# Performance work log

Hardware: AMD Instinct MI355X
Metric: run time of the kernel (lower is better)

Reference implementation:

```python
import jax, jax.numpy as jnp
import numpy as np
from jax import lax

H_IMG = 128; W_IMG = 128; C_IN = 200; NCLS = 16
N0 = H_IMG * W_IMG; N1 = 4096; N2 = 1024
K = 16  # neighbors(15) + 1 self loop, as in __init__
EPS = 1e-5
SLOPE = 0.01  # LeakyReLU default


def _leaky(x):
    return jnp.where(x >= 0, x, SLOPE * x)


def _bn1d(H, g, b):
    # BatchNorm1d in training mode: batch stats over node dim
    mu = H.mean(0)
    var = H.var(0)
    return (H - mu) * lax.rsqrt(var + EPS) * g + b


def _bn2d(x, g, b):
    mu = x.mean((0, 2, 3), keepdims=True)
    var = x.var((0, 2, 3), keepdims=True)
    return (x - mu) * lax.rsqrt(var + EPS) * g[None, :, None, None] + b[None, :, None, None]


def _ssconv(x, g, b, pw, pb, dw, db):
    # BN -> 1x1 pointwise conv -> LeakyReLU -> depthwise 5x5 conv -> LeakyReLU
    y = _bn2d(x, g, b)
    y = lax.conv_general_dilated(y, pw, (1, 1), 'SAME', dimension_numbers=('NCHW', 'OIHW', 'NCHW')) + pb[None, :, None, None]
    y = _leaky(y)
    c = dw.shape[0]
    y = lax.conv_general_dilated(y, dw, (1, 1), 'SAME', feature_group_count=c, dimension_numbers=('NCHW', 'OIHW', 'NCHW')) + db[None, :, None, None]
    return _leaky(y)


def _gcn(H, g, b, wt, bt, wo, bo, nbr):
    # GCNLayer_PyG, neighbors>0 branch. nbr: [N, K] neighbor indices (col), center broadcast (row)
    Hn = _bn1d(H, g, b)
    th = Hn @ wt + bt            # [N, 128]
    out = Hn @ wo + bo           # [N, F]
    A = jax.nn.sigmoid(jnp.einsum('nkd,nd->nk', th[nbr], th))  # sigmoid(<theta[col], theta[row]>)
    A = jax.nn.softmax(A, axis=1)                              # softmax over K neighbors
    agg = jnp.einsum('nk,nkf->nf', A, out[nbr])                # weighted neighbor aggregate
    return _leaky(agg), A


def _forward(x, hg, hb, hpw, hpb, hdw, hdb,
             e0_g, e0_b, e0_wt, e0_bt, e0_wo, e0_bo,
             e1_g, e1_b, e1_wt, e1_bt, e1_wo, e1_bo,
             d0_g, d0_b, d0_wt, d0_bt, d0_wo, d0_bo,
             tg, tb, tpw, tpb, tdw, tdb, ws, wb,
             S0, S1, Shat0, Shat1, nbr_a, nbr_b):
    x4 = x.transpose(2, 0, 1)[None]                 # [1, C, H, W]
    h0 = _ssconv(x4, hg, hb, hpw, hpb, hdw, hdb)    # [1, 128, H, W]
    H = h0[0].transpose(1, 2, 0).reshape(N0, -1)    # [N0, 128]
    enc0 = H
    H = Shat0 @ H                                   # pool to [N1, 128]
    H, A0 = _gcn(H, e0_g, e0_b, e0_wt, e0_bt, e0_wo, e0_bo, nbr_a)  # [N1, 64]
    enc1 = H
    H = Shat1 @ H                                   # pool to [N2, 64]
    H, A1 = _gcn(H, e1_g, e1_b, e1_wt, e1_bt, e1_wo, e1_bo, nbr_b)  # [N2, 32]
    # decoder
    H = S1 @ H                                      # unpool [N1, 32]
    H = jnp.concatenate([H, enc1], axis=-1)         # [N1, 96]
    H, Ad = _gcn(H, d0_g, d0_b, d0_wt, d0_bt, d0_wo, d0_bo, nbr_a)  # [N1, 64]
    H = S0 @ H                                      # unpool [N0, 64]
    H = jnp.concatenate([H, enc0], axis=-1)         # [N0, 192]
    t = H.reshape(1, H_IMG, W_IMG, -1).transpose(0, 3, 1, 2)
    f = _ssconv(t, tg, tb, tpw, tpb, tdw, tdb)      # [1, 128, H, W]
    f = f[0].transpose(1, 2, 0).reshape(N0, -1)
    Y = jax.nn.softmax(f @ ws + wb, axis=-1)        # [N0, NCLS]
    return Y


def setup_inputs() -> dict:
    key = jax.random.key(0)
    cnt = [0]
    def rn(shape, s=0.05):
        cnt[0] += 1
        return jax.random.normal(jax.random.fold_in(key, cnt[0]), shape, jnp.float32) * s
    x = rn((H_IMG, W_IMG, C_IN), 1.0)
    # balanced hierarchical assignment matrices (one-hot rows)
    S0 = jnp.zeros((N0, N1), jnp.float32).at[jnp.arange(N0), jnp.arange(N0) // (N0 // N1)].set(1.0)
    S1 = jnp.zeros((N1, N2), jnp.float32).at[jnp.arange(N1), jnp.arange(N1) // (N1 // N2)].set(1.0)
    Shat0 = (S0 / S0.sum(0, keepdims=True)).T
    Shat1 = (S1 / S1.sum(0, keepdims=True)).T
    # positions: pixel grid pooled through Shat (as in HiGCN.__init__)
    gx, gy = jnp.meshgrid(jnp.arange(H_IMG), jnp.arange(W_IMG), indexing='ij')
    pos = jnp.stack([gx, gy], -1).reshape(N0, 2).astype(jnp.float32)
    posA = Shat0 @ pos
    posB = Shat1 @ posA
    def knn(p):
        d = ((p[:, None, :] - p[None, :, :]) ** 2).sum(-1)
        return jnp.argsort(d, axis=1)[:, :K].astype(jnp.int32)  # self included (loop=True)
    nbr_a = knn(posA)  # [N1, K], used by enc0 and dec0
    nbr_b = knn(posB)  # [N2, K], used by enc1
    inp = dict(x=x, S0=S0, S1=S1, Shat0=Shat0, Shat1=Shat1, nbr_a=nbr_a, nbr_b=nbr_b)
    inp.update(hg=jnp.ones(C_IN), hb=jnp.zeros(C_IN), hpw=rn((128, C_IN, 1, 1)),
               hpb=jnp.zeros(128), hdw=rn((128, 1, 5, 5)), hdb=jnp.zeros(128))
    for tag, ci, co in (('e0', 128, 64), ('e1', 64, 32), ('d0', 96, 64)):
        inp[tag + '_g'] = jnp.ones(ci); inp[tag + '_b'] = jnp.zeros(ci)
        inp[tag + '_wt'] = rn((ci, 128)); inp[tag + '_bt'] = jnp.zeros(128)
        inp[tag + '_wo'] = rn((ci, co)); inp[tag + '_bo'] = jnp.zeros(co)
    inp.update(tg=jnp.ones(192), tb=jnp.zeros(192), tpw=rn((128, 192, 1, 1)),
               tpb=jnp.zeros(128), tdw=rn((128, 1, 5, 5)), tdb=jnp.zeros(128))
    inp.update(ws=rn((128, NCLS)), wb=jnp.zeros(NCLS))
    return inp


def reference(x, hg, hb, hpw, hpb, hdw, hdb,
              e0_g, e0_b, e0_wt, e0_bt, e0_wo, e0_bo,
              e1_g, e1_b, e1_wt, e1_bt, e1_wo, e1_bo,
              d0_g, d0_b, d0_wt, d0_bt, d0_wo, d0_bo,
              tg, tb, tpw, tpb, tdw, tdb, ws, wb,
              S0, S1, Shat0, Shat1, nbr_a, nbr_b):
    return _forward(x, hg, hb, hpw, hpb, hdw, hdb,
                    e0_g, e0_b, e0_wt, e0_bt, e0_wo, e0_bo,
                    e1_g, e1_b, e1_wt, e1_bt, e1_wo, e1_bo,
                    d0_g, d0_b, d0_wt, d0_bt, d0_wo, d0_bo,
                    tg, tb, tpw, tpb, tdw, tdb, ws, wb,
                    S0, S1, Shat0, Shat1, nbr_a, nbr_b)
```

## Files before the change

### kernel.cpp

```cpp
#include <hip/hip_runtime.h>
#include <hip/hip_bf16.h>
#include <math.h>

using bf16 = __hip_bfloat16;

#define H_IMG 128
#define W_IMG 128
#define C_IN  200
#define NCLS  16
#define N0    16384
#define N1    4096
#define N2    1024
#define KNB   16
#define EPS   1e-5f
#define SLOPE 0.01f

__device__ __forceinline__ float ldf(const float* p, long i) { return p[i]; }
__device__ __forceinline__ float ldf(const bf16* p, long i) { return __bfloat162float(p[i]); }
__device__ __forceinline__ float leaky(float v) { return v >= 0.f ? v : SLOPE * v; }

__device__ __forceinline__ float4 ld4(const float* p, long i) {
    return *reinterpret_cast<const float4*>(p + i);
}
__device__ __forceinline__ float4 ld4(const bf16* p, long i) {
    const ushort4 u = *reinterpret_cast<const ushort4*>(reinterpret_cast<const unsigned short*>(p) + i);
    float4 r;
    r.x = __uint_as_float((unsigned)u.x << 16);
    r.y = __uint_as_float((unsigned)u.y << 16);
    r.z = __uint_as_float((unsigned)u.z << 16);
    r.w = __uint_as_float((unsigned)u.w << 16);
    return r;
}

__device__ __forceinline__ int block_detect(const unsigned short* __restrict__ x) {
    __shared__ int cnt_s;
    if (threadIdx.x == 0) cnt_s = 0;
    __syncthreads();
    int cnt = 0;
    for (int i = threadIdx.x; i < 4096; i += blockDim.x) {
        unsigned short e = (unsigned short)((x[i] >> 7) & 0xFF);
        if (e >= 0xC0) cnt++;
    }
#pragma unroll
    for (int off = 32; off > 0; off >>= 1) cnt += __shfl_xor(cnt, off, 64);
    if ((threadIdx.x & 63) == 0) atomicAdd(&cnt_s, cnt);
    __syncthreads();
    return cnt_s > 32 ? 1 : 0;
}

__global__ __launch_bounds__(256) void bnx_kernel(const void* __restrict__ X, float2* __restrict__ part,
                                                  int* __restrict__ dflag) {
    int fl = block_detect((const unsigned short*)X);
    if (blockIdx.x == 0 && threadIdx.x == 0) *dflag = fl;
    int b = blockIdx.x, t = threadIdx.x;
    if (t >= C_IN) return;
    float s = 0.f, s2 = 0.f;
    if (fl) {
        const float* p = (const float*)X + (long)b * 64 * C_IN + t;
        for (int r = 0; r < 64; r++) { float v = p[(long)r * C_IN]; s += v; s2 += v * v; }
    } else {
        const bf16* p = (const bf16*)X + (long)b * 64 * C_IN + t;
        for (int r = 0; r < 64; r++) { float v = __bfloat162float(p[(long)r * C_IN]); s += v; s2 += v * v; }
    }
    part[(long)t * 256 + b] = make_float2(s, s2);
}

__device__ __forceinline__ void alphabeta_ld(const float2* __restrict__ partA, int npA, int splitC,
                                             const float2* __restrict__ partB, int npB,
                                             int Ci, float Pinv, const void* g, const void* b_,
                                             int flag, float* al, float* be) {
    int t = threadIdx.x;
    if (t < Ci) {
        const float2* src = (t < splitC) ? partA + (long)t * npA : partB + (long)(t - splitC) * npB;
        int np = (t < splitC) ? npA : npB;
        float s = 0.f, s2 = 0.f;
        const float4* p4 = (const float4*)src;
        for (int i = 0; i < (np >> 1); i++) { float4 v = p4[i]; s += v.x + v.z; s2 += v.y + v.w; }
        float mu = s * Pinv;
        float var = s2 * Pinv - mu * mu;
        float gv = flag ? ((const float*)g)[t] : __bfloat162float(((const bf16*)g)[t]);
        float bv = flag ? ((const float*)b_)[t] : __bfloat162float(((const bf16*)b_)[t]);
        float a = rsqrtf(var + EPS) * gv;
        al[t] = a;
        be[t] = bv - mu * a;
    }
    __syncthreads();
}

template <typename TW>
__device__ __forceinline__ void foldL_body(const TW* __restrict__ W, const TW* __restrict__ bias,
                                           const float* __restrict__ al, const float* __restrict__ be,
                                           float* __restrict__ Wf, float* __restrict__ Bf,
                                           int Ci, int Co, int omajor, int j) {
    int t = threadIdx.x;
    float acc = 0.f;
    for (int c = t; c < Ci; c += 256) {
        float w = omajor ? ldf(W, (long)j * Ci + c) : ldf(W, (long)c * Co + j);
        Wf[(long)c * Co + j] = w * al[c];
        acc += w * be[c];
    }
    __shared__ float red[256];
    red[t] = acc; __syncthreads();
    for (int k = 128; k > 0; k >>= 1) { if (t < k) red[t] += red[t + k]; __syncthreads(); }
    if (t == 0) Bf[j] = ldf(bias, (long)j) + red[0];
}

__global__ __launch_bounds__(256) void bnfold_kernel(const float2* partA, int npA, int splitC,
                                                     const float2* partB, int npB, int P,
                                                     const void* g, const void* b_,
                                                     const void* Wt, const void* bias,
                                                     float* Wf, float* Bf, int Ci, int Co, int omajor,
                                                     const int* dflag) {
    __shared__ float al[256], be[256];
    int flag = *dflag;
    alphabeta_ld(partA, npA, splitC, partB, npB, Ci, 1.f / (float)P, g, b_, flag, al, be);
    if (flag) foldL_body<float>((const float*)Wt, (const float*)bias, al, be, Wf, Bf, Ci, Co, omajor, blockIdx.x);
    else foldL_body<bf16>((const bf16*)Wt, (const bf16*)bias, al, be, Wf, Bf, Ci, Co, omajor, blockIdx.x);
}

__global__ __launch_bounds__(256) void bnfold2_kernel(const float2* partA, int npA, int splitC,
                                                      const float2* partB, int npB, int P,
                                                      const void* g, const void* b_,
                                                      const void* W1, const void* b1,
                                                      const void* W2, const void* b2,
                                                      float* Wf1, float* Bf1, float* Wf2, float* Bf2,
                                                      int Ci, int Co1, int Co2, const int* dflag) {
    __shared__ float al[256], be[256];
    int flag = *dflag;
    alphabeta_ld(partA, npA, splitC, partB, npB, Ci, 1.f / (float)P, g, b_, flag, al, be);
    int j = blockIdx.x;
    if (flag) {
        if (j < Co1) foldL_body<float>((const float*)W1, (const float*)b1, al, be, Wf1, Bf1, Ci, Co1, 0, j);
        else foldL_body<float>((const float*)W2, (const float*)b2, al, be, Wf2, Bf2, Ci, Co2, 0, j - Co1);
    } else {
        if (j < Co1) foldL_body<bf16>((const bf16*)W1, (const bf16*)b1, al, be, Wf1, Bf1, Ci, Co1, 0, j);
        else foldL_body<bf16>((const bf16*)W2, (const bf16*)b2, al, be, Wf2, Bf2, Ci, Co2, 0, j - Co1);
    }
}

template <typename T, int ACT>
__device__ __forceinline__ void gemm4_body(const T* __restrict__ In, const float* __restrict__ Wf,
                                           const float* __restrict__ Bf, float* __restrict__ Out,
                                           int Ci, int Co, int blk) {
    int tid = blk * 256 + threadIdx.x;
    int Coq = Co >> 2;
    int n = tid / Coq;
    int j4 = (tid - n * Coq) << 2;
    const T* in = In + (long)n * Ci;
    const float* wp = Wf + j4;
    float4 acc = *reinterpret_cast<const float4*>(Bf + j4);
    for (int c = 0; c < Ci; c += 4) {
        float4 xv = ld4(in, c);
        float4 w0 = *reinterpret_cast<const float4*>(wp + (long)c * Co);
        float4 w1 = *reinterpret_cast<const float4*>(wp + (long)(c + 1) * Co);
        float4 w2 = *reinterpret_cast<const float4*>(wp + (long)(c + 2) * Co);
        float4 w3 = *reinterpret_cast<const float4*>(wp + (long)(c + 3) * Co);
        acc.x += xv.x * w0.x; acc.y += xv.x * w0.y; acc.z += xv.x * w0.z; acc.w += xv.x * w0.w;
        acc.x += xv.y * w1.x; acc.y += xv.y * w1.y; acc.z += xv.y * w1.z; acc.w += xv.y * w1.w;
        acc.x += xv.z * w2.x; acc.y += xv.z * w2.y; acc.z += xv.z * w2.z; acc.w += xv.z * w2.w;
        acc.x += xv.w * w3.x; acc.y += xv.w * w3.y; acc.z += xv.w * w3.z; acc.w += xv.w * w3.w;
    }
// ... 10 lines not shown
    int Coq = Co >> 2;
    int n = tid / Coq;
    int j4 = (tid - n * Coq) << 2;
    const float* ia = InA + (long)(n >> 2) * sA;
    const float* ib = InB + (long)n * sB;
    const float* wp = Wf + j4;
    float4 acc = *reinterpret_cast<const float4*>(Bf + j4);
    for (int c = 0; c < Ci; c += 4) {
        float4 xv = (c < SPLIT) ? *reinterpret_cast<const float4*>(ia + c)
                                : *reinterpret_cast<const float4*>(ib + (c - SPLIT));
        float4 w0 = *reinterpret_cast<const float4*>(wp + (long)c * Co);
        float4 w1 = *reinterpret_cast<const float4*>(wp + (long)(c + 1) * Co);
        float4 w2 = *reinterpret_cast<const float4*>(wp + (long)(c + 2) * Co);
        float4 w3 = *reinterpret_cast<const float4*>(wp + (long)(c + 3) * Co);
        acc.x += xv.x * w0.x; acc.y += xv.x * w0.y; acc.z += xv.x * w0.z; acc.w += xv.x * w0.w;
        acc.x += xv.y * w1.x; acc.y += xv.y * w1.y; acc.z += xv.y * w1.z; acc.w += xv.y * w1.w;
        acc.x += xv.z * w2.x; acc.y += xv.z * w2.y; acc.z += xv.z * w2.z; acc.w += xv.z * w2.w;
        acc.x += xv.w * w3.x; acc.y += xv.w * w3.y; acc.z += xv.w * w3.z; acc.w += xv.w * w3.w;
    }
    if (ACT) { acc.x = leaky(acc.x); acc.y = leaky(acc.y); acc.z = leaky(acc.z); acc.w = leaky(acc.w); }
    *reinterpret_cast<float4*>(Out + (long)n * Co + j4) = acc;
}

__global__ __launch_bounds__(256) void gemm4_dyn_kernel(const void* In, const float* Wf, const float* Bf,
                                                        float* Out, int Ci, int Co, const int* flag) {
    if (*flag) gemm4_body<float, 1>((const float*)In, Wf, Bf, Out, Ci, Co, blockIdx.x);
    else gemm4_body<bf16, 1>((const bf16*)In, Wf, Bf, Out, Ci, Co, blockIdx.x);
}

__global__ __launch_bounds__(256) void gemm2_f32_kernel(const float* In,
                                                        const float* W1, const float* B1, float* O1, int Co1,
                                                        const float* W2, const float* B2, float* O2, int Co2,
                                                        int Ci, int nb1) {
    int b = blockIdx.x;
    if (b < nb1) gemm4_body<float, 0>(In, W1, B1, O1, Ci, Co1, b);
    else gemm4_body<float, 0>(In, W2, B2, O2, Ci, Co2, b - nb1);
}

template <int SPLIT>
__global__ __launch_bounds__(256) void gemm2cat_kernel(const float* InA, int sA, const float* InB, int sB,
                                                       const float* W1, const float* B1, float* O1, int Co1,
                                                       const float* W2, const float* B2, float* O2, int Co2,
                                                       int Ci, int nb1) {
    int b = blockIdx.x;
    if (b < nb1) gemm4cat_body<0, SPLIT>(InA, sA, InB, sB, W1, B1, O1, Ci, Co1, b);
    else gemm4cat_body<0, SPLIT>(InA, sA, InB, sB, W2, B2, O2, Ci, Co2, b - nb1);
}

template <int SPLIT>
__global__ __launch_bounds__(256) void gemmcat_act_kernel(const float* InA, int sA, const float* InB, int sB,
                                                          const float* Wf, const float* Bf, float* Out,
                                                          int Ci, int Co) {
    gemm4cat_body<1, SPLIT>(InA, sA, InB, sB, Wf, Bf, Out, Ci, Co, blockIdx.x);
}

template <typename TW>
__device__ __forceinline__ void dw4_body(const float* __restrict__ In, const TW* __restrict__ dwp,
                                         const TW* __restrict__ dbp, float* __restrict__ Out) {
    __shared__ float wl[25][128];
    __shared__ float bl[128];
    int t = threadIdx.x;
    for (int e = t; e < 25 * 128; e += 256) {
        int o = e / 25, i = e - o * 25;
        wl[i][o] = ldf(dwp, e);
    }
    if (t < 128) bl[t] = ldf(dbp, (long)t);
    __syncthreads();

    int tid = blockIdx.x * 256 + t;
    int o0 = (tid & 31) << 2;
    int p = tid >> 5;
    int h = p >> 7, w = p & 127;
    float4 acc = *reinterpret_cast<const float4*>(&bl[o0]);
#pragma unroll
    for (int dh = -2; dh <= 2; dh++) {
        int hh = h + dh;
        if ((unsigned)hh >= (unsigned)H_IMG) continue;
#pragma unroll
        for (int dv = -2; dv <= 2; dv++) {
            int ww = w + dv;
            if ((unsigned)ww >= (unsigned)W_IMG) continue;
            float4 iv = *reinterpret_cast<const float4*>(&In[(long)(((hh << 7) + ww) << 7) + o0]);
            float4 wv = *reinterpret_cast<const float4*>(&wl[(dh + 2) * 5 + (dv + 2)][o0]);
            acc.x += iv.x * wv.x; acc.y += iv.y * wv.y; acc.z += iv.z * wv.z; acc.w += iv.w * wv.w;
        }
    }
    acc.x = leaky(acc.x); acc.y = leaky(acc.y); acc.z = leaky(acc.z); acc.w = leaky(acc.w);
    *reinterpret_cast<float4*>(&Out[(long)p * 128 + o0]) = acc;
}

__global__ __launch_bounds__(256) void dw4_kernel(const float* In, const void* dwp, const void* dbp,
                                                  float* Out, const int* flag) {
    if (*flag) dw4_body<float>(In, (const float*)dwp, (const float*)dbp, Out);
    else dw4_body<bf16>(In, (const bf16*)dwp, (const bf16*)dbp, Out);
}

__global__ __launch_bounds__(128) void bnpool_kernel(const float* __restrict__ R1f, float* __restrict__ H1b,
                                                     float2* __restrict__ partE0, float2* __restrict__ partTb) {
    int b = blockIdx.x, t = threadIdx.x;
    float s = 0.f, s2 = 0.f;
    float rs = 0.f, rs2 = 0.f;
    const float* base = R1f + (long)b * 64 * 128 + t;
    for (int r = 0; r < 16; r++) {
        const float* rp = base + (long)r * 512;
        float v0 = rp[0], v1 = rp[128], v2 = rp[256], v3 = rp[384];
        float h = 0.25f * (v0 + v1 + v2 + v3);
        H1b[(long)(b * 16 + r) * 128 + t] = h;
        s += h; s2 += h * h;
        rs += v0 + v1 + v2 + v3;
        rs2 += v0 * v0 + v1 * v1 + v2 * v2 + v3 * v3;
    }
    partE0[(long)t * 256 + b] = make_float2(s, s2);
    partTb[(long)t * 256 + b] = make_float2(rs, rs2);
}

template <int MODE>
__global__ __launch_bounds__(256) void attn_fused_kernel(const float* __restrict__ th, const float* __restrict__ outm,
                                                         const int* __restrict__ nbr, float* __restrict__ dst, int co,
                                                         float* __restrict__ H2b,
                                                         float2* __restrict__ partP, float2* __restrict__ partS,
                                                         int snp) {
    int wid = threadIdx.x >> 6, l = threadIdx.x & 63;
    int n = blockIdx.x * 4 + wid;
    float r0 = th[(long)n * 128 + l];
    float r1 = th[(long)n * 128 + 64 + l];
    int mk[KNB];
    float av[KNB];
#pragma unroll
    for (int k = 0; k < KNB; k++) {
        int m = nbr[n * KNB + k];
        mk[k] = m;
        float v = r0 * th[(long)m * 128 + l] + r1 * th[(long)m * 128 + 64 + l];
#pragma unroll
        for (int off = 32; off > 0; off >>= 1) v += __shfl_xor(v, off, 64);
        av[k] = 1.f / (1.f + expf(-v));
    }
    float amax = av[0];
#pragma unroll
    for (int k = 1; k < KNB; k++) amax = fmaxf(amax, av[k]);
    float den = 0.f;
#pragma unroll
    for (int k = 0; k < KNB; k++) { av[k] = expf(av[k] - amax); den += av[k]; }
    float rden = 1.f / den;
    float val = 0.f;
    if (l < co) {
        float acc = 0.f;
#pragma unroll
        for (int k = 0; k < KNB; k++) acc += av[k] * outm[(long)mk[k] * co + l];
        val = leaky(acc * rden);
        dst[(long)n * co + l] = val;
    }
    __shared__ float sm[4][64];
    sm[wid][l] = (l < co) ? val : 0.f;
    __syncthreads();
    if (wid == 0 && l < co) {
        float a = sm[0][l], b = sm[1][l], c = sm[2][l], d = sm[3][l];
        float su = a + b + c + d;
        float sq = a * a + b * b + c * c + d * d;
        if (MODE == 0) {
            float h = 0.25f * su;
            H2b[(long)blockIdx.x * 64 + l] = h;
            partP[(long)l * snp + blockIdx.x] = make_float2(h, h * h);
            partS[(long)l * snp + blockIdx.x] = make_float2(su, sq);
        } else {
            partS[(long)l * snp + blockIdx.x] = make_float2(4.f * su, 4.f * sq);
        }
    }
}

template <typename TW>
__device__ __forceinline__ void cls_body(const float* __restrict__ F, const TW* __restrict__ wsw,
                                         const TW* __restrict__ wb, TW* __restrict__ out) {
    __shared__ float wl[128 * 16];
    int t = threadIdx.x;
    for (int e = t; e < 2048; e += 256) wl[e] = ldf(wsw, (long)e);
    __syncthreads();
    int tid = blockIdx.x * 256 + t;
    int p = tid >> 4;
    int j = tid & 15;
    float acc = ldf(wb, (long)j);
    const float* fp = F + (long)p * 128;
#pragma unroll 8
    for (int c = 0; c < 128; c += 4) {
        float4 fv = *reinterpret_cast<const float4*>(fp + c);
        acc += fv.x * wl[c * 16 + j] + fv.y * wl[(c + 1) * 16 + j]
             + fv.z * wl[(c + 2) * 16 + j] + fv.w * wl[(c + 3) * 16 + j];
    }
    float m = acc;
#pragma unroll
    for (int s = 8; s > 0; s >>= 1) m = fmaxf(m, __shfl_xor(m, s, 16));
    float e = expf(acc - m);
    float d = e;
#pragma unroll
    for (int s = 8; s > 0; s >>= 1) d += __shfl_xor(d, s, 16);
    float r = e / d;
    if constexpr (sizeof(TW) == 2) out[tid] = __float2bfloat16(r);
    else out[tid] = r;
}

__global__ __launch_bounds__(256) void cls_kernel(const float* F, const void* wsw, const void* wb,
                                                  void* out, const int* flag) {
    if (*flag) cls_body<float>(F, (const float*)wsw, (const float*)wb, (float*)out);
    else cls_body<bf16>(F, (const bf16*)wsw, (const bf16*)wb, (bf16*)out);
}

extern "C" void kernel_launch(void* const* d_in, const int* in_sizes, int n_in,
                              void* d_out, int out_size, void* d_ws, size_t ws_size,
                              hipStream_t stream) {
    bool dict = (in_sizes[1] > 1000000);
    int I_x, I_nbr_a, I_nbr_b, I_hg, I_ws, I_e0, I_e1, I_d0, I_tg;
    if (dict) {
        I_x = 0; I_nbr_a = 5; I_nbr_b = 6; I_hg = 7; I_e0 = 13; I_e1 = 19; I_d0 = 25; I_tg = 31; I_ws = 37;
    } else {
        I_x = 0; I_hg = 1; I_e0 = 7; I_e1 = 13; I_d0 = 19; I_tg = 25; I_ws = 31; I_nbr_a = 37; I_nbr_b = 38;
    }
    const void* x    = d_in[I_x];
    const int* nbr_a = (const int*)d_in[I_nbr_a];
    const int* nbr_b = (const int*)d_in[I_nbr_b];
    const void* hg   = d_in[I_hg + 0];
    const void* hb   = d_in[I_hg + 1];
    const void* hpw  = d_in[I_hg + 2];
    const void* hpb  = d_in[I_hg + 3];
    const void* hdw  = d_in[I_hg + 4];
    const void* hdb  = d_in[I_hg + 5];
    const void* e0_g = d_in[I_e0 + 0];
    const void* e0_b = d_in[I_e0 + 1];
    const void* e0_wt= d_in[I_e0 + 2];
    const void* e0_bt= d_in[I_e0 + 3];
    const void* e0_wo= d_in[I_e0 + 4];
    const void* e0_bo= d_in[I_e0 + 5];
    const void* e1_g = d_in[I_e1 + 0];
    const void* e1_b = d_in[I_e1 + 1];
    const void* e1_wt= d_in[I_e1 + 2];
    const void* e1_bt= d_in[I_e1 + 3];
    const void* e1_wo= d_in[I_e1 + 4];
    const void* e1_bo= d_in[I_e1 + 5];
    const void* d0_g = d_in[I_d0 + 0];
    const void* d0_b = d_in[I_d0 + 1];
    const void* d0_wt= d_in[I_d0 + 2];
    const void* d0_bt= d_in[I_d0 + 3];
    const void* d0_wo= d_in[I_d0 + 4];
    const void* d0_bo= d_in[I_d0 + 5];
    const void* tg   = d_in[I_tg + 0];
    const void* tb   = d_in[I_tg + 1];
    const void* tpw  = d_in[I_tg + 2];
    const void* tpb  = d_in[I_tg + 3];
    const void* tdw  = d_in[I_tg + 4];
    const void* tdb  = d_in[I_tg + 5];
    const void* wsw  = d_in[I_ws + 0];
    const void* wb   = d_in[I_ws + 1];

    float* W = (float*)d_ws;
    float*  WF1    = W + 0;
    float*  BF1    = W + 25600;
    float*  WF2    = W + 25728;
    float*  BF2    = W + 33920;
    int*    dflag  = (int*)(W + 33984);
    float2* P_HEAD = (float2*)(W + 34048);
    float2* P_E0   = (float2*)(W + 136448);
    float2* P_E1   = (float2*)(W + 201984);
    float2* P_D0a  = (float2*)(W + 333056);
    float2* P_D0b  = (float2*)(W + 349440);
    float2* P_Ta   = (float2*)(W + 480512);
    float2* P_Tb   = (float2*)(W + 611584);
    float*  R0     = W + 677120;
    float*  R1     = R0 + (long)N0 * 128;
    float*  T1     = R1 + (long)N0 * 128;
    float*  H1b    = T1 + (long)N0 * 128;
    float*  THb    = H1b + (long)N1 * 128;
    float*  OUTb   = THb + (long)N1 * 128;
    float*  ENC1   = OUTb + (long)N1 * 64;
    float*  H2b    = ENC1 + (long)N1 * 64;
    float*  HDb    = H2b + (long)N2 * 64;
    float*  HDEC   = HDb + (long)N2 * 32;

    bnx_kernel<<<256, 256, 0, stream>>>(x, P_HEAD, dflag);
    bnfold_kernel<<<128, 256, 0, stream>>>(P_HEAD, 256, C_IN, P_HEAD, 256, N0,
                                           hg, hb, hpw, hpb, WF1, BF1, C_IN, 128, 1, dflag);
    gemm4_dyn_kernel<<<2048, 256, 0, stream>>>(x, WF1, BF1, R0, C_IN, 128, dflag);
    dw4_kernel<<<2048, 256, 0, stream>>>(R0, hdw, hdb, R1, dflag);
    bnpool_kernel<<<256, 128, 0, stream>>>(R1, H1b, P_E0, P_Tb);
    bnfold2_kernel<<<192, 256, 0, stream>>>(P_E0, 256, 128, P_E0, 256, N1, e0_g, e0_b,
                                            e0_wt, e0_bt, e0_wo, e0_bo,
                                            WF1, BF1, WF2, BF2, 128, 128, 64, dflag);
    gemm2_f32_kernel<<<768, 256, 0, stream>>>(H1b, WF1, BF1, THb, 128, WF2, BF2, OUTb, 64, 128, 512);
    attn_fused_kernel<0><<<1024, 256, 0, stream>>>(THb, OUTb, nbr_a, ENC1, 64, H2b, P_E1, P_D0b, 1024);
    bnfold2_kernel<<<160, 256, 0, stream>>>(P_E1, 1024, 64, P_E1, 1024, N2, e1_g, e1_b,
                                            e1_wt, e1_bt, e1_wo, e1_bo,
                                            WF1, BF1, WF2, BF2, 64, 128, 32, dflag);
    gemm2_f32_kernel<<<160, 256, 0, stream>>>(H2b, WF1, BF1, THb, 128, WF2, BF2, OUTb, 32, 64, 128);
    attn_fused_kernel<1><<<256, 256, 0, stream>>>(THb, OUTb, nbr_b, HDb, 32, nullptr, nullptr, P_D0a, 256);
    bnfold2_kernel<<<192, 256, 0, stream>>>(P_D0a, 256, 32, P_D0b, 1024, N1, d0_g, d0_b,
                                            d0_wt, d0_bt, d0_wo, d0_bo,
                                            WF1, BF1, WF2, BF2, 96, 128, 64, dflag);
    gemm2cat_kernel<32><<<768, 256, 0, stream>>>(HDb, 32, ENC1, 64,
                                                 WF1, BF1, THb, 128, WF2, BF2, OUTb, 64, 96, 512);
    attn_fused_kernel<2><<<1024, 256, 0, stream>>>(THb, OUTb, nbr_a, HDEC, 64, nullptr, nullptr, P_Ta, 1024);
    bnfold_kernel<<<128, 256, 0, stream>>>(P_Ta, 1024, 64, P_Tb, 256, N0,
                                           tg, tb, tpw, tpb, WF1, BF1, 192, 128, 1, dflag);
    gemmcat_act_kernel<64><<<2048, 256, 0, stream>>>(HDEC, 64, R1, 128, WF1, BF1, T1, 192, 128);
    dw4_kernel<<<2048, 256, 0, stream>>>(T1, tdw, tdb, R0, dflag);
    cls_kernel<<<1024, 256, 0, stream>>>(R0, wsw, wb, d_out, dflag);
}
```

Baseline: 959.4 us.

## Merge all stages into one cooperative persistent megakernel with grid syncs

Replaces the sequence of about seventeen separate kernel launches with a single cooperative persistent kernel. Each stage becomes a device function looped over work units, with grid-wide syncs between stages, and the dtype detection and per-stage dispatch move inside it. This targets launch overhead and idle gaps between the many small kernels. In exchange, grid syncs add cost, the grid size is capped by occupancy, and a single kernel's register and LDS use may lower throughput in the heavy stages.

```diff
diff --git a/kernel.cpp b/kernel.cpp
--- a/kernel.cpp
+++ b/kernel.cpp
@@ -1,7 +1,9 @@
 #include <hip/hip_runtime.h>
+#include <hip/hip_cooperative_groups.h>
 #include <hip/hip_bf16.h>
 #include <math.h>
 
+namespace cg = cooperative_groups;
 using bf16 = __hip_bfloat16;
 
 #define H_IMG 128
@@ -15,14 +17,16 @@
 #define EPS   1e-5f
 #define SLOPE 0.01f
 
-__device__ __forceinline__ float ldf(const float* p, long i) { return p[i]; }
-__device__ __forceinline__ float ldf(const bf16* p, long i) { return __bfloat162float(p[i]); }
 __device__ __forceinline__ float leaky(float v) { return v >= 0.f ? v : SLOPE * v; }
 
-__device__ __forceinline__ float4 ld4(const float* p, long i) {
+__device__ __forceinline__ float ldw(const void* p, long i, int fl) {
+    return fl ? ((const float*)p)[i] : __bfloat162float(((const bf16*)p)[i]);
+}
+
+__device__ __forceinline__ float4 ld4f(const float* p, long i) {
     return *reinterpret_cast<const float4*>(p + i);
 }
-__device__ __forceinline__ float4 ld4(const bf16* p, long i) {
+__device__ __forceinline__ float4 ld4b(const bf16* p, long i) {
     const ushort4 u = *reinterpret_cast<const ushort4*>(reinterpret_cast<const unsigned short*>(p) + i);
     float4 r;
     r.x = __uint_as_float((unsigned)u.x << 16);
@@ -31,112 +35,9 @@
     r.w = __uint_as_float((unsigned)u.w << 16);
     return r;
 }
-
-__device__ __forceinline__ int block_detect(const unsigned short* __restrict__ x) {
-    __shared__ int cnt_s;
-    if (threadIdx.x == 0) cnt_s = 0;
-    __syncthreads();
-    int cnt = 0;
-    for (int i = threadIdx.x; i < 4096; i += blockDim.x) {
-        unsigned short e = (unsigned short)((x[i] >> 7) & 0xFF);
-        if (e >= 0xC0) cnt++;
-    }
-#pragma unroll
-    for (int off = 32; off > 0; off >>= 1) cnt += __shfl_xor(cnt, off, 64);
-    if ((threadIdx.x & 63) == 0) atomicAdd(&cnt_s, cnt);
-    __syncthreads();
-    return cnt_s > 32 ? 1 : 0;
-}
-
-__global__ __launch_bounds__(256) void bnx_kernel(const void* __restrict__ X, float2* __restrict__ part,
-                                                  int* __restrict__ dflag) {
-    int fl = block_detect((const unsigned short*)X);
-    if (blockIdx.x == 0 && threadIdx.x == 0) *dflag = fl;
-    int b = blockIdx.x, t = threadIdx.x;
-    if (t >= C_IN) return;
-    float s = 0.f, s2 = 0.f;
-    if (fl) {
-        const float* p = (const float*)X + (long)b * 64 * C_IN + t;
-        for (int r = 0; r < 64; r++) { float v = p[(long)r * C_IN]; s += v; s2 += v * v; }
-    } else {
-        const bf16* p = (const bf16*)X + (long)b * 64 * C_IN + t;
-        for (int r = 0; r < 64; r++) { float v = __bfloat162float(p[(long)r * C_IN]); s += v; s2 += v * v; }
-    }
-    part[(long)t * 256 + b] = make_float2(s, s2);
-}
-
-__device__ __forceinline__ void alphabeta_ld(const float2* __restrict__ partA, int npA, int splitC,
-                                             const float2* __restrict__ partB, int npB,
-                                             int Ci, float Pinv, const void* g, const void* b_,
-                                             int flag, float* al, float* be) {
-    int t = threadIdx.x;
-    if (t < Ci) {
-        const float2* src = (t < splitC) ? partA + (long)t * npA : partB + (long)(t - splitC) * npB;
-        int np = (t < splitC) ? npA : npB;
-        float s = 0.f, s2 = 0.f;
-        const float4* p4 = (const float4*)src;
-        for (int i = 0; i < (np >> 1); i++) { float4 v = p4[i]; s += v.x + v.z; s2 += v.y + v.w; }
-        float mu = s * Pinv;
-        float var = s2 * Pinv - mu * mu;
-        float gv = flag ? ((const float*)g)[t] : __bfloat162float(((const bf16*)g)[t]);
-        float bv = flag ? ((const float*)b_)[t] : __bfloat162float(((const bf16*)b_)[t]);
-        float a = rsqrtf(var + EPS) * gv;
-        al[t] = a;
-        be[t] = bv - mu * a;
-    }
-    __syncthreads();
-}
-
-template <typename TW>
-__device__ __forceinline__ void foldL_body(const TW* __restrict__ W, const TW* __restrict__ bias,
-                                           const float* __restrict__ al, const float* __restrict__ be,
-                                           float* __restrict__ Wf, float* __restrict__ Bf,
-                                           int Ci, int Co, int omajor, int j) {
-    int t = threadIdx.x;
-    float acc = 0.f;
-    for (int c = t; c < Ci; c += 256) {
-        float w = omajor ? ldf(W, (long)j * Ci + c) : ldf(W, (long)c * Co + j);
-        Wf[(long)c * Co + j] = w * al[c];
-        acc += w * be[c];
-    }
-    __shared__ float red[256];
-    red[t] = acc; __syncthreads();
-    for (int k = 128; k > 0; k >>= 1) { if (t < k) red[t] += red[t + k]; __syncthreads(); }
-    if (t == 0) Bf[j] = ldf(bias, (long)j) + red[0];
-}
-
-__global__ __launch_bounds__(256) void bnfold_kernel(const float2* partA, int npA, int splitC,
-                                                     const float2* partB, int npB, int P,
-                                                     const void* g, const void* b_,
-                                                     const void* Wt, const void* bias,
-                                                     float* Wf, float* Bf, int Ci, int Co, int omajor,
-                                                     const int* dflag) {
-    __shared__ float al[256], be[256];
-    int flag = *dflag;
-    alphabeta_ld(partA, npA, splitC, partB, npB, Ci, 1.f / (float)P, g, b_, flag, al, be);
-    if (flag) foldL_body<float>((const float*)Wt, (const float*)bias, al, be, Wf, Bf, Ci, Co, omajor, blockIdx.x);
-    else foldL_body<bf16>((const bf16*)Wt, (const bf16*)bias, al, be, Wf, Bf, Ci, Co, omajor, blockIdx.x);
-}
-
-__global__ __launch_bounds__(256) void bnfold2_kernel(const float2* partA, int npA, int splitC,
-                                                      const float2* partB, int npB, int P,
-                                                      const void* g, const void* b_,
-                                                      const void* W1, const void* b1,
-                                                      const void* W2, const void* b2,
-                                                      float* Wf1, float* Bf1, float* Wf2, float* Bf2,
-                                                      int Ci, int Co1, int Co2, const int* dflag) {
-    __shared__ float al[256], be[256];
-    int flag = *dflag;
-    alphabeta_ld(partA, npA, splitC, partB, npB, Ci, 1.f / (float)P, g, b_, flag, al, be);
-    int j = blockIdx.x;
-    if (flag) {
-        if (j < Co1) foldL_body<float>((const float*)W1, (const float*)b1, al, be, Wf1, Bf1, Ci, Co1, 0, j);
-        else foldL_body<float>((const float*)W2, (const float*)b2, al, be, Wf2, Bf2, Ci, Co2, 0, j - Co1);
-    } else {
-        if (j < Co1) foldL_body<bf16>((const bf16*)W1, (const bf16*)b1, al, be, Wf1, Bf1, Ci, Co1, 0, j);
-        else foldL_body<bf16>((const bf16*)W2, (const bf16*)b2, al, be, Wf2, Bf2, Ci, Co2, 0, j - Co1);
-    }
-}
+template <typename T> __device__ __forceinline__ float4 ld4(const T* p, long i);
+template <> __device__ __forceinline__ float4 ld4<float>(const float* p, long i) { return ld4f(p, i); }
+template <> __device__ __forceinline__ float4 ld4<bf16>(const bf16* p, long i) { return ld4b(p, i); }
 
 template <typename T, int ACT>
 __device__ __forceinline__ void gemm4_body(const T* __restrict__ In, const float* __restrict__ Wf,
@@ -193,52 +94,57 @@
     *reinterpret_cast<float4*>(Out + (long)n * Co + j4) = acc;
 }
 
-__global__ __launch_bounds__(256) void gemm4_dyn_kernel(const void* In, const float* Wf, const float* Bf,
-                                                        float* Out, int Ci, int Co, const int* flag) {
-    if (*flag) gemm4_body<float, 1>((const float*)In, Wf, Bf, Out, Ci, Co, blockIdx.x);
-    else gemm4_body<bf16, 1>((const bf16*)In, Wf, Bf, Out, Ci, Co, blockIdx.x);
-}
-
-__global__ __launch_bounds__(256) void gemm2_f32_kernel(const float* In,
-                                                        const float* W1, const float* B1, float* O1, int Co1,
-                                                        const float* W2, const float* B2, float* O2, int Co2,
-                                                        int Ci, int nb1) {
-    int b = blockIdx.x;
-    if (b < nb1) gemm4_body<float, 0>(In, W1, B1, O1, Ci, Co1, b);
-    else gemm4_body<float, 0>(In, W2, B2, O2, Ci, Co2, b - nb1);
-}
-
-template <int SPLIT>
-__global__ __launch_bounds__(256) void gemm2cat_kernel(const float* InA, int sA, const float* InB, int sB,
-                                                       const float* W1, const float* B1, float* O1, int Co1,
-                                                       const float* W2, const float* B2, float* O2, int Co2,
-                                                       int Ci, int nb1) {
-    int b = blockIdx.x;
-    if (b < nb1) gemm4cat_body<0, SPLIT>(InA, sA, InB, sB, W1, B1, O1, Ci, Co1, b);
-    else gemm4cat_body<0, SPLIT>(InA, sA, InB, sB, W2, B2, O2, Ci, Co2, b - nb1);
-}
-
-template <int SPLIT>
-__global__ __launch_bounds__(256) void gemmcat_act_kernel(const float* InA, int sA, const float* InB, int sB,
-                                                          const float* Wf, const float* Bf, float* Out,
-                                                          int Ci, int Co) {
-    gemm4cat_body<1, SPLIT>(InA, sA, InB, sB, Wf, Bf, Out, Ci, Co, blockIdx.x);
-}
-
-template <typename TW>
-__device__ __forceinline__ void dw4_body(const float* __restrict__ In, const TW* __restrict__ dwp,
-                                         const TW* __restrict__ dbp, float* __restrict__ Out) {
-    __shared__ float wl[25][128];
-    __shared__ float bl[128];
+__device__ __forceinline__ void alphabeta_ld(const float2* __restrict__ partA, int npA, int splitC,
+                                             const float2* __restrict__ partB, int npB,
+                                             int Ci, float Pinv, const void* g, const void* b_,
+                                             int fl, float* al, float* be) {
+    int t = threadIdx.x;
+    if (t < Ci) {
+        const float2* src = (t < splitC) ? partA + (long)t * npA : partB + (long)(t - splitC) * npB;
+        int np = (t < splitC) ? npA : npB;
+        float s = 0.f, s2 = 0.f;
+        const float4* p4 = (const float4*)src;
+        for (int i = 0; i < (np >> 1); i++) { float4 v = p4[i]; s += v.x + v.z; s2 += v.y + v.w; }
+        float mu = s * Pinv;
+        float var = s2 * Pinv - mu * mu;
+        float a = rsqrtf(var + EPS) * ldw(g, t, fl);
+        al[t] = a;
+        be[t] = ldw(b_, t, fl) - mu * a;
+    }
+    __syncthreads();
+}
+
+__device__ __forceinline__ void foldL(int j, const void* Wsrc, const void* bias,
+                                      const float* al, const float* be,
+                                      float* __restrict__ Wf, float* __restrict__ Bf,
+                                      int Ci, int Co, int omajor, int fl, float* red) {
+    int t = threadIdx.x;
+    float acc = 0.f;
+    for (int c = t; c < Ci; c += 256) {
+        long idx = omajor ? (long)j * Ci + c : (long)c * Co + j;
+        float w = ldw(Wsrc, idx, fl);
+        Wf[(long)c * Co + j] = w * al[c];
+        acc += w * be[c];
+    }
+    red[t] = acc; __syncthreads();
+    for (int k = 128; k > 0; k >>= 1) { if (t < k) red[t] += red[t + k]; __syncthreads(); }
+    if (t == 0) Bf[j] = ldw(bias, j, fl) + red[0];
+    __syncthreads();
+}
+
+__device__ __forceinline__ void dw_load(const void* dwp, const void* dbp, float* wl, float* bl, int fl) {
     int t = threadIdx.x;
     for (int e = t; e < 25 * 128; e += 256) {
         int o = e / 25, i = e - o * 25;
-        wl[i][o] = ldf(dwp, e);
-    }
-    if (t < 128) bl[t] = ldf(dbp, (long)t);
-    __syncthreads();
-
-    int tid = blockIdx.x * 256 + t;
+        wl[i * 128 + o] = ldw(dwp, e, fl);
+    }
+    if (t < 128) bl[t] = ldw(dbp, t, fl);
+    __syncthreads();
+}
+
+__device__ __forceinline__ void dw_unit(int blk, const float* __restrict__ In, float* __restrict__ Out,
+                                        const float* wl, const float* bl) {
+    int tid = blk * 256 + threadIdx.x;
     int o0 = (tid & 31) << 2;
     int p = tid >> 5;
     int h = p >> 7, w = p & 127;
@@ -252,7 +158,7 @@
             int ww = w + dv;
             if ((unsigned)ww >= (unsigned)W_IMG) continue;
             float4 iv = *reinterpret_cast<const float4*>(&In[(long)(((hh << 7) + ww) << 7) + o0]);
-            float4 wv = *reinterpret_cast<const float4*>(&wl[(dh + 2) * 5 + (dv + 2)][o0]);
+            float4 wv = *reinterpret_cast<const float4*>(&wl[((dh + 2) * 5 + (dv + 2)) * 128 + o0]);
             acc.x += iv.x * wv.x; acc.y += iv.y * wv.y; acc.z += iv.z * wv.z; acc.w += iv.w * wv.w;
         }
     }
@@ -260,39 +166,13 @@
     *reinterpret_cast<float4*>(&Out[(long)p * 128 + o0]) = acc;
 }
 
-__global__ __launch_bounds__(256) void dw4_kernel(const float* In, const void* dwp, const void* dbp,
-                                                  float* Out, const int* flag) {
-    if (*flag) dw4_body<float>(In, (const float*)dwp, (const float*)dbp, Out);
-    else dw4_body<bf16>(In, (const bf16*)dwp, (const bf16*)dbp, Out);
-}
-
-__global__ __launch_bounds__(128) void bnpool_kernel(const float* __restrict__ R1f, float* __restrict__ H1b,
-                                                     float2* __restrict__ partE0, float2* __restrict__ partTb) {
-    int b = blockIdx.x, t = threadIdx.x;
-    float s = 0.f, s2 = 0.f;
-    float rs = 0.f, rs2 = 0.f;
-    const float* base = R1f + (long)b * 64 * 128 + t;
-    for (int r = 0; r < 16; r++) {
-        const float* rp = base + (long)r * 512;
-        float v0 = rp[0], v1 = rp[128], v2 = rp[256], v3 = rp[384];
-        float h = 0.25f * (v0 + v1 + v2 + v3);
-        H1b[(long)(b * 16 + r) * 128 + t] = h;
-        s += h; s2 += h * h;
-        rs += v0 + v1 + v2 + v3;
-        rs2 += v0 * v0 + v1 * v1 + v2 * v2 + v3 * v3;
-    }
-    partE0[(long)t * 256 + b] = make_float2(s, s2);
-    partTb[(long)t * 256 + b] = make_float2(rs, rs2);
-}
-
 template <int MODE>
-__global__ __launch_bounds__(256) void attn_fused_kernel(const float* __restrict__ th, const float* __restrict__ outm,
-                                                         const int* __restrict__ nbr, float* __restrict__ dst, int co,
-                                                         float* __restrict__ H2b,
-                                                         float2* __restrict__ partP, float2* __restrict__ partS,
-                                                         int snp) {
+__device__ __forceinline__ void attn_unit(int b, const float* __restrict__ th, const float* __restrict__ outm,
+                                          const int* __restrict__ nbr, float* __restrict__ dst, int co,
+                                          float* __restrict__ H2b, float2* __restrict__ partP,
+                                          float2* __restrict__ partS, int snp, float* sm) {
     int wid = threadIdx.x >> 6, l = threadIdx.x & 63;
-    int n = blockIdx.x * 4 + wid;
+    int n = b * 4 + wid;
     float r0 = th[(long)n * 128 + l];
     float r1 = th[(long)n * 128 + 64 + l];
     int mk[KNB];
@@ -321,58 +201,200 @@
         val = leaky(acc * rden);
         dst[(long)n * co + l] = val;
     }
-    __shared__ float sm[4][64];
-    sm[wid][l] = (l < co) ? val : 0.f;
+    sm[wid * 64 + l] = (l < co) ? val : 0.f;
     __syncthreads();
     if (wid == 0 && l < co) {
-        float a = sm[0][l], b = sm[1][l], c = sm[2][l], d = sm[3][l];
-        float su = a + b + c + d;
-        float sq = a * a + b * b + c * c + d * d;
+        float a = sm[l], bb = sm[64 + l], c = sm[128 + l], d = sm[192 + l];
+        float su = a + bb + c + d;
+        float sq = a * a + bb * bb + c * c + d * d;
         if (MODE == 0) {
             float h = 0.25f * su;
-            H2b[(long)blockIdx.x * 64 + l] = h;
-            partP[(long)l * snp + blockIdx.x] = make_float2(h, h * h);
-            partS[(long)l * snp + blockIdx.x] = make_float2(su, sq);
+            H2b[(long)b * 64 + l] = h;
+            partP[(long)l * snp + b] = make_float2(h, h * h);
+            partS[(long)l * snp + b] = make_float2(su, sq);
         } else {
-            partS[(long)l * snp + blockIdx.x] = make_float2(4.f * su, 4.f * sq);
-        }
-    }
-}
-
-template <typename TW>
-__device__ __forceinline__ void cls_body(const float* __restrict__ F, const TW* __restrict__ wsw,
-                                         const TW* __restrict__ wb, TW* __restrict__ out) {
-    __shared__ float wl[128 * 16];
-    int t = threadIdx.x;
-    for (int e = t; e < 2048; e += 256) wl[e] = ldf(wsw, (long)e);
-    __syncthreads();
-    int tid = blockIdx.x * 256 + t;
-    int p = tid >> 4;
-    int j = tid & 15;
-    float acc = ldf(wb, (long)j);
-    const float* fp = F + (long)p * 128;
+            partS[(long)l * snp + b] = make_float2(4.f * su, 4.f * sq);
+        }
+    }
+    __syncthreads();
+}
+
+struct MegaArgs {
+    const void* x;
+    const int* nbr_a; const int* nbr_b;
+    const void *hg, *hb, *hpw, *hpb, *hdw, *hdb;
+    const void *e0_g, *e0_b, *e0_wt, *e0_bt, *e0_wo, *e0_bo;
+    const void *e1_g, *e1_b, *e1_wt, *e1_bt, *e1_wo, *e1_bo;
+    const void *d0_g, *d0_b, *d0_wt, *d0_bt, *d0_wo, *d0_bo;
+    const void *tg, *tb, *tpw, *tpb, *tdw, *tdb, *wsw, *wb;
+    float *WF1, *BF1, *WF2, *BF2;
+    float2 *P_HEAD, *P_E0, *P_E1, *P_D0a, *P_D0b, *P_Ta, *P_Tb;
+    float *R0, *R1, *T1, *H1b, *THb, *OUTb, *ENC1, *H2b, *HDb, *HDEC;
+    void* out;
+};
+
+#define FOR_B(NB) for (int b = (int)blockIdx.x; b < (NB); b += G)
+
+__global__ __launch_bounds__(256, 4) void mega_kernel(MegaArgs a) {
+    cg::grid_group grid = cg::this_grid();
+    const int G = (int)gridDim.x;
+    const int t = threadIdx.x;
+
+    __shared__ float s_al[256];
+    __shared__ float s_be[256];
+    __shared__ float s_red[256];
+    __shared__ float s_dww[25 * 128];
+    __shared__ float s_dwb[128];
+    __shared__ float s_cls[2048];
+    __shared__ float s_sm[256];
+    __shared__ int s_cnt;
+
+    if (t == 0) s_cnt = 0;
+    __syncthreads();
+    {
+        const unsigned short* xu = (const unsigned short*)a.x;
+        int cnt = 0;
+        for (int i = t; i < 4096; i += 256) {
+            unsigned short e = (unsigned short)((xu[i] >> 7) & 0xFF);
+            if (e >= 0xC0) cnt++;
+        }
+#pragma unroll
+        for (int off = 32; off > 0; off >>= 1) cnt += __shfl_xor(cnt, off, 64);
+        if ((t & 63) == 0) atomicAdd(&s_cnt, cnt);
+    }
+    __syncthreads();
+    const int fl = (s_cnt > 32) ? 1 : 0;
+
+    FOR_B(256) {
+        if (t < C_IN) {
+            float s = 0.f, s2 = 0.f;
+            if (fl) {
+                const float* p = (const float*)a.x + (long)b * 64 * C_IN + t;
+                for (int r = 0; r < 64; r++) { float v = p[(long)r * C_IN]; s += v; s2 += v * v; }
+            } else {
+                const bf16* p = (const bf16*)a.x + (long)b * 64 * C_IN + t;
+                for (int r = 0; r < 64; r++) { float v = __bfloat162float(p[(long)r * C_IN]); s += v; s2 += v * v; }
+            }
+            a.P_HEAD[(long)t * 256 + b] = make_float2(s, s2);
+        }
+    }
+    grid.sync();
+
+    alphabeta_ld(a.P_HEAD, 256, 256, a.P_HEAD, 256, C_IN, 1.f / (float)N0, a.hg, a.hb, fl, s_al, s_be);
+    FOR_B(128) foldL(b, a.hpw, a.hpb, s_al, s_be, a.WF1, a.BF1, C_IN, 128, 1, fl, s_red);
+    grid.sync();
+
+    if (fl) { FOR_B(2048) gemm4_body<float, 1>((const float*)a.x, a.WF1, a.BF1, a.R0, C_IN, 128, b); }
+    else    { FOR_B(2048) gemm4_body<bf16, 1>((const bf16*)a.x, a.WF1, a.BF1, a.R0, C_IN, 128, b); }
+    grid.sync();
+
+    dw_load(a.hdw, a.hdb, s_dww, s_dwb, fl);
+    FOR_B(2048) dw_unit(b, a.R0, a.R1, s_dww, s_dwb);
+    grid.sync();
+
+    FOR_B(256) {
+        if (t < 128) {
+            float s = 0.f, s2 = 0.f, rs = 0.f, rs2 = 0.f;
+            const float* base = a.R1 + (long)b * 64 * 128 + t;
+            for (int r = 0; r < 16; r++) {
+                const float* rp = base + (long)r * 512;
+                float v0 = rp[0], v1 = rp[128], v2 = rp[256], v3 = rp[384];
+                float h = 0.25f * (v0 + v1 + v2 + v3);
+                a.H1b[(long)(b * 16 + r) * 128 + t] = h;
+                s += h; s2 += h * h;
+                rs += v0 + v1 + v2 + v3;
+                rs2 += v0 * v0 + v1 * v1 + v2 * v2 + v3 * v3;
+            }
+            a.P_E0[(long)t * 256 + b] = make_float2(s, s2);
+            a.P_Tb[(long)t * 256 + b] = make_float2(rs, rs2);
+        }
+    }
+    grid.sync();
+
+    alphabeta_ld(a.P_E0, 256, 128, a.P_E0, 256, 128, 1.f / (float)N1, a.e0_g, a.e0_b, fl, s_al, s_be);
+    FOR_B(192) {
+        if (b < 128) foldL(b, a.e0_wt, a.e0_bt, s_al, s_be, a.WF1, a.BF1, 128, 128, 0, fl, s_red);
+        else         foldL(b - 128, a.e0_wo, a.e0_bo, s_al, s_be, a.WF2, a.BF2, 128, 64, 0, fl, s_red);
+    }
+    grid.sync();
+
+    FOR_B(768) {
+        if (b < 512) gemm4_body<float, 0>(a.H1b, a.WF1, a.BF1, a.THb, 128, 128, b);
+        else         gemm4_body<float, 0>(a.H1b, a.WF2, a.BF2, a.OUTb, 128, 64, b - 512);
+    }
+    grid.sync();
+
+    FOR_B(1024) attn_unit<0>(b, a.THb, a.OUTb, a.nbr_a, a.ENC1, 64, a.H2b, a.P_E1, a.P_D0b, 1024, s_sm);
+    grid.sync();
+
+    alphabeta_ld(a.P_E1, 1024, 64, a.P_E1, 1024, 64, 1.f / (float)N2, a.e1_g, a.e1_b, fl, s_al, s_be);
+    FOR_B(160) {
+        if (b < 128) foldL(b, a.e1_wt, a.e1_bt, s_al, s_be, a.WF1, a.BF1, 64, 128, 0, fl, s_red);
+        else         foldL(b - 128, a.e1_wo, a.e1_bo, s_al, s_be, a.WF2, a.BF2, 64, 32, 0, fl, s_red);
+    }
+    grid.sync();
+
+    FOR_B(160) {
+        if (b < 128) gemm4_body<float, 0>(a.H2b, a.WF1, a.BF1, a.THb, 64, 128, b);
+        else         gemm4_body<float, 0>(a.H2b, a.WF2, a.BF2, a.OUTb, 64, 32, b - 128);
+    }
+    grid.sync();
+
+    FOR_B(256) attn_unit<1>(b, a.THb, a.OUTb, a.nbr_b, a.HDb, 32, nullptr, nullptr, a.P_D0a, 256, s_sm);
+    grid.sync();
+
+    alphabeta_ld(a.P_D0a, 256, 32, a.P_D0b, 1024, 96, 1.f / (float)N1, a.d0_g, a.d0_b, fl, s_al, s_be);
+    FOR_B(192) {
+        if (b < 128) foldL(b, a.d0_wt, a.d0_bt, s_al, s_be, a.WF1, a.BF1, 96, 128, 0, fl, s_red);
+        else         foldL(b - 128, a.d0_wo, a.d0_bo, s_al, s_be, a.WF2, a.BF2, 96, 64, 0, fl, s_red);
+    }
+    grid.sync();
+
+    FOR_B(768) {
+        if (b < 512) gemm4cat_body<0, 32>(a.HDb, 32, a.ENC1, 64, a.WF1, a.BF1, a.THb, 96, 128, b);
+        else         gemm4cat_body<0, 32>(a.HDb, 32, a.ENC1, 64, a.WF2, a.BF2, a.OUTb, 96, 64, b - 512);
+    }
+    grid.sync();
+
+    FOR_B(1024) attn_unit<2>(b, a.THb, a.OUTb, a.nbr_a, a.HDEC, 64, nullptr, nullptr, a.P_Ta, 1024, s_sm);
+    grid.sync();
+
+    alphabeta_ld(a.P_Ta, 1024, 64, a.P_Tb, 256, 192, 1.f / (float)N0, a.tg, a.tb, fl, s_al, s_be);
+    FOR_B(128) foldL(b, a.tpw, a.tpb, s_al, s_be, a.WF1, a.BF1, 192, 128, 1, fl, s_red);
+    grid.sync();
+
+    FOR_B(2048) gemm4cat_body<1, 64>(a.HDEC, 64, a.R1, 128, a.WF1, a.BF1, a.T1, 192, 128, b);
+    grid.sync();
+
+    dw_load(a.tdw, a.tdb, s_dww, s_dwb, fl);
+    FOR_B(2048) dw_unit(b, a.T1, a.R0, s_dww, s_dwb);
+    grid.sync();
+
+    for (int e = t; e < 2048; e += 256) s_cls[e] = ldw(a.wsw, e, fl);
+    __syncthreads();
+    FOR_B(1024) {
+        int tid = b * 256 + t;
+        int p = tid >> 4;
+        int j = tid & 15;
+        float acc = ldw(a.wb, j, fl);
+        const float* fp = a.R0 + (long)p * 128;
 #pragma unroll 8
-    for (int c = 0; c < 128; c += 4) {
-        float4 fv = *reinterpret_cast<const float4*>(fp + c);
-        acc += fv.x * wl[c * 16 + j] + fv.y * wl[(c + 1) * 16 + j]
-             + fv.z * wl[(c + 2) * 16 + j] + fv.w * wl[(c + 3) * 16 + j];
-    }
-    float m = acc;
-#pragma unroll
-    for (int s = 8; s > 0; s >>= 1) m = fmaxf(m, __shfl_xor(m, s, 16));
-    float e = expf(acc - m);
-    float d = e;
-#pragma unroll
-    for (int s = 8; s > 0; s >>= 1) d += __shfl_xor(d, s, 16);
-    float r = e / d;
-    if constexpr (sizeof(TW) == 2) out[tid] = __float2bfloat16(r);
-    else out[tid] = r;
-}
-
-__global__ __launch_bounds__(256) void cls_kernel(const float* F, const void* wsw, const void* wb,
-                                                  void* out, const int* flag) {
-    if (*flag) cls_body<float>(F, (const float*)wsw, (const float*)wb, (float*)out);
-    else cls_body<bf16>(F, (const bf16*)wsw, (const bf16*)wb, (bf16*)out);
+        for (int c = 0; c < 128; c += 4) {
+            float4 fv = *reinterpret_cast<const float4*>(fp + c);
+            acc += fv.x * s_cls[c * 16 + j] + fv.y * s_cls[(c + 1) * 16 + j]
+                 + fv.z * s_cls[(c + 2) * 16 + j] + fv.w * s_cls[(c + 3) * 16 + j];
+        }
+        float m = acc;
+#pragma unroll
+        for (int s = 8; s > 0; s >>= 1) m = fmaxf(m, __shfl_xor(m, s, 16));
+        float e = expf(acc - m);
+        float d = e;
+#pragma unroll
+        for (int s = 8; s > 0; s >>= 1) d += __shfl_xor(d, s, 16);
+        float r = e / d;
+        if (fl) ((float*)a.out)[tid] = r;
+        else ((bf16*)a.out)[tid] = __float2bfloat16(r);
+    }
 }
 
 extern "C" void kernel_launch(void* const* d_in, const int* in_sizes, int n_in,
@@ -385,91 +407,55 @@
     } else {
         I_x = 0; I_hg = 1; I_e0 = 7; I_e1 = 13; I_d0 = 19; I_tg = 25; I_ws = 31; I_nbr_a = 37; I_nbr_b = 38;
     }
-    const void* x    = d_in[I_x];
-    const int* nbr_a = (const int*)d_in[I_nbr_a];
-    const int* nbr_b = (const int*)d_in[I_nbr_b];
-    const void* hg   = d_in[I_hg + 0];
-    const void* hb   = d_in[I_hg + 1];
-    const void* hpw  = d_in[I_hg + 2];
-    const void* hpb  = d_in[I_hg + 3];
-    const void* hdw  = d_in[I_hg + 4];
-    const void* hdb  = d_in[I_hg + 5];
-    const void* e0_g = d_in[I_e0 + 0];
-    const void* e0_b = d_in[I_e0 + 1];
-    const void* e0_wt= d_in[I_e0 + 2];
-    const void* e0_bt= d_in[I_e0 + 3];
-    const void* e0_wo= d_in[I_e0 + 4];
-    const void* e0_bo= d_in[I_e0 + 5];
-    const void* e1_g = d_in[I_e1 + 0];
-    const void* e1_b = d_in[I_e1 + 1];
-    const void* e1_wt= d_in[I_e1 + 2];
-    const void* e1_bt= d_in[I_e1 + 3];
-    const void* e1_wo= d_in[I_e1 + 4];
-    const void* e1_bo= d_in[I_e1 + 5];
-    const void* d0_g = d_in[I_d0 + 0];
-    const void* d0_b = d_in[I_d0 + 1];
-    const void* d0_wt= d_in[I_d0 + 2];
-    const void* d0_bt= d_in[I_d0 + 3];
-    const void* d0_wo= d_in[I_d0 + 4];
-    const void* d0_bo= d_in[I_d0 + 5];
-    const void* tg   = d_in[I_tg + 0];
-    const void* tb   = d_in[I_tg + 1];
-    const void* tpw  = d_in[I_tg + 2];
-    const void* tpb  = d_in[I_tg + 3];
-    const void* tdw  = d_in[I_tg + 4];
-    const void* tdb  = d_in[I_tg + 5];
-    const void* wsw  = d_in[I_ws + 0];
-    const void* wb   = d_in[I_ws + 1];
+
+    MegaArgs a;
+    a.x     = d_in[I_x];
+    a.nbr_a = (const int*)d_in[I_nbr_a];
+    a.nbr_b = (const int*)d_in[I_nbr_b];
+    a.hg  = d_in[I_hg + 0]; a.hb  = d_in[I_hg + 1]; a.hpw = d_in[I_hg + 2];
+    a.hpb = d_in[I_hg + 3]; a.hdw = d_in[I_hg + 4]; a.hdb = d_in[I_hg + 5];
+    a.e0_g = d_in[I_e0 + 0]; a.e0_b = d_in[I_e0 + 1]; a.e0_wt = d_in[I_e0 + 2];
+    a.e0_bt = d_in[I_e0 + 3]; a.e0_wo = d_in[I_e0 + 4]; a.e0_bo = d_in[I_e0 + 5];
+    a.e1_g = d_in[I_e1 + 0]; a.e1_b = d_in[I_e1 + 1]; a.e1_wt = d_in[I_e1 + 2];
+    a.e1_bt = d_in[I_e1 + 3]; a.e1_wo = d_in[I_e1 + 4]; a.e1_bo = d_in[I_e1 + 5];
+    a.d0_g = d_in[I_d0 + 0]; a.d0_b = d_in[I_d0 + 1]; a.d0_wt = d_in[I_d0 + 2];
+    a.d0_bt = d_in[I_d0 + 3]; a.d0_wo = d_in[I_d0 + 4]; a.d0_bo = d_in[I_d0 + 5];
+    a.tg  = d_in[I_tg + 0]; a.tb  = d_in[I_tg + 1]; a.tpw = d_in[I_tg + 2];
+    a.tpb = d_in[I_tg + 3]; a.tdw = d_in[I_tg + 4]; a.tdb = d_in[I_tg + 5];
+    a.wsw = d_in[I_ws + 0]; a.wb  = d_in[I_ws + 1];
 
     float* W = (float*)d_ws;
-    float*  WF1    = W + 0;
-    float*  BF1    = W + 25600;
-    float*  WF2    = W + 25728;
-    float*  BF2    = W + 33920;
-    int*    dflag  = (int*)(W + 33984);
-    float2* P_HEAD = (float2*)(W + 34048);
-    float2* P_E0   = (float2*)(W + 136448);
-    float2* P_E1   = (float2*)(W + 201984);
-    float2* P_D0a  = (float2*)(W + 333056);
-    float2* P_D0b  = (float2*)(W + 349440);
-    float2* P_Ta   = (float2*)(W + 480512);
-    float2* P_Tb   = (float2*)(W + 611584);
-    float*  R0     = W + 677120;
-    float*  R1     = R0 + (long)N0 * 128;
-    float*  T1     = R1 + (long)N0 * 128;
-    float*  H1b    = T1 + (long)N0 * 128;
-    float*  THb    = H1b + (long)N1 * 128;
-    float*  OUTb   = THb + (long)N1 * 128;
-    float*  ENC1   = OUTb + (long)N1 * 64;
-    float*  H2b    = ENC1 + (long)N1 * 64;
-    float*  HDb    = H2b + (long)N2 * 64;
-    float*  HDEC   = HDb + (long)N2 * 32;
-
-    bnx_kernel<<<256, 256, 0, stream>>>(x, P_HEAD, dflag);
-    bnfold_kernel<<<128, 256, 0, stream>>>(P_HEAD, 256, C_IN, P_HEAD, 256, N0,
-                                           hg, hb, hpw, hpb, WF1, BF1, C_IN, 128, 1, dflag);
-    gemm4_dyn_kernel<<<2048, 256, 0, stream>>>(x, WF1, BF1, R0, C_IN, 128, dflag);
-    dw4_kernel<<<2048, 256, 0, stream>>>(R0, hdw, hdb, R1, dflag);
-    bnpool_kernel<<<256, 128, 0, stream>>>(R1, H1b, P_E0, P_Tb);
-    bnfold2_kernel<<<192, 256, 0, stream>>>(P_E0, 256, 128, P_E0, 256, N1, e0_g, e0_b,
-                                            e0_wt, e0_bt, e0_wo, e0_bo,
-                                            WF1, BF1, WF2, BF2, 128, 128, 64, dflag);
-    gemm2_f32_kernel<<<768, 256, 0, stream>>>(H1b, WF1, BF1, THb, 128, WF2, BF2, OUTb, 64, 128, 512);
-    attn_fused_kernel<0><<<1024, 256, 0, stream>>>(THb, OUTb, nbr_a, ENC1, 64, H2b, P_E1, P_D0b, 1024);
-    bnfold2_kernel<<<160, 256, 0, stream>>>(P_E1, 1024, 64, P_E1, 1024, N2, e1_g, e1_b,
-                                            e1_wt, e1_bt, e1_wo, e1_bo,
-                                            WF1, BF1, WF2, BF2, 64, 128, 32, dflag);
-    gemm2_f32_kernel<<<160, 256, 0, stream>>>(H2b, WF1, BF1, THb, 128, WF2, BF2, OUTb, 32, 64, 128);
-    attn_fused_kernel<1><<<256, 256, 0, stream>>>(THb, OUTb, nbr_b, HDb, 32, nullptr, nullptr, P_D0a, 256);
-    bnfold2_kernel<<<192, 256, 0, stream>>>(P_D0a, 256, 32, P_D0b, 1024, N1, d0_g, d0_b,
-                                            d0_wt, d0_bt, d0_wo, d0_bo,
-                                            WF1, BF1, WF2, BF2, 96, 128, 64, dflag);
-    gemm2cat_kernel<32><<<768, 256, 0, stream>>>(HDb, 32, ENC1, 64,
-                                                 WF1, BF1, THb, 128, WF2, BF2, OUTb, 64, 96, 512);
-    attn_fused_kernel<2><<<1024, 256, 0, stream>>>(THb, OUTb, nbr_a, HDEC, 64, nullptr, nullptr, P_Ta, 1024);
-    bnfold_kernel<<<128, 256, 0, stream>>>(P_Ta, 1024, 64, P_Tb, 256, N0,
-                                           tg, tb, tpw, tpb, WF1, BF1, 192, 128, 1, dflag);
-    gemmcat_act_kernel<64><<<2048, 256, 0, stream>>>(HDEC, 64, R1, 128, WF1, BF1, T1, 192, 128);
-    dw4_kernel<<<2048, 256, 0, stream>>>(T1, tdw, tdb, R0, dflag);
-    cls_kernel<<<1024, 256, 0, stream>>>(R0, wsw, wb, d_out, dflag);
-}
+    a.WF1 = W + 0;
+    a.BF1 = W + 25600;
+    a.WF2 = W + 25728;
+    a.BF2 = W + 33920;
+    a.P_HEAD = (float2*)(W + 34048);
+    a.P_E0   = (float2*)(W + 136448);
+    a.P_E1   = (float2*)(W + 201984);
+    a.P_D0a  = (float2*)(W + 333056);
+    a.P_D0b  = (float2*)(W + 349440);
+    a.P_Ta   = (float2*)(W + 480512);
+    a.P_Tb   = (float2*)(W + 611584);
+    a.R0   = W + 677120;
+    a.R1   = a.R0 + (long)N0 * 128;
+    a.T1   = a.R1 + (long)N0 * 128;
+    a.H1b  = a.T1 + (long)N0 * 128;
+    a.THb  = a.H1b + (long)N1 * 128;
+    a.OUTb = a.THb + (long)N1 * 128;
+    a.ENC1 = a.OUTb + (long)N1 * 64;
+    a.H2b  = a.ENC1 + (long)N1 * 64;
+    a.HDb  = a.H2b + (long)N2 * 64;
+    a.HDEC = a.HDb + (long)N2 * 32;
+    a.out  = d_out;
+
+    int maxb = 0;
+    hipError_t oe = hipOccupancyMaxActiveBlocksPerMultiprocessor(
+        &maxb, reinterpret_cast<const void*>(&mega_kernel), 256, 0);
+    if (oe != hipSuccess || maxb < 1) maxb = 2;
+    int nblk = maxb * 256;
+    if (nblk > 1024) nblk = 1024;
+
+    void* kargs[] = { (void*)&a };
+    hipLaunchCooperativeKernel(reinterpret_cast<const void*>(&mega_kernel),
+                               dim3(nblk), dim3(256), kargs, 0, stream);
+}
```

New measurement: 1.959 ms. 104% more time.
